# Optimization experiments

Hardware: AMD Instinct MI355X
Metric: run time of the kernel (lower is better)

The kernel has to match this reference:

```python
import jax, jax.numpy as jnp
import numpy as np

N = 100000   # nodes
E = 640000   # edges
F = 128      # num_features
D = 128      # dim
G = 128      # graphs in batch
BN_EPS = 1e-5


def setup_inputs() -> dict:
    key = jax.random.key(0)
    ks = jax.random.split(key, 16)
    lin = lambda k, i, o: (jax.random.normal(k, (i, o), jnp.float32) / np.sqrt(i)).astype(jnp.float32)
    inp = {
        "x": jax.random.normal(ks[0], (N, F), jnp.float32),
        "edge_index": jax.random.randint(ks[1], (2, E), 0, N),
        "batch": jnp.sort(jax.random.randint(ks[2], (N,), 0, G)),
        # layer 0: Linear(F,D)-ReLU-Linear(D,D), BN(D)
        "W0a": lin(ks[3], F, D), "b0a": jnp.zeros((D,), jnp.float32),
        "W0b": lin(ks[4], D, D), "b0b": jnp.zeros((D,), jnp.float32),
        "g0": jnp.ones((D,), jnp.float32), "be0": jnp.zeros((D,), jnp.float32),
        # layer 1: Linear(D,D)-ReLU-Linear(D,D), BN(D)
        "W1a": lin(ks[5], D, D), "b1a": jnp.zeros((D,), jnp.float32),
        "W1b": lin(ks[6], D, D), "b1b": jnp.zeros((D,), jnp.float32),
        "g1": jnp.ones((D,), jnp.float32), "be1": jnp.zeros((D,), jnp.float32),
        # layer 2: Linear(D,D)-ReLU-Linear(D,1), BN(1)
        "W2a": lin(ks[7], D, D), "b2a": jnp.zeros((D,), jnp.float32),
        "W2b": lin(ks[8], D, 1), "b2b": jnp.zeros((1,), jnp.float32),
        "g2": jnp.ones((1,), jnp.float32), "be2": jnp.zeros((1,), jnp.float32),
    }
    return inp


def _gin_layer(x, src, dst, Wa, ba, Wb, bb, g, be, relu_out):
    # GINConv (eps=0): h = x + sum_{j in N(i)} x_j, then MLP, then BN (train-mode stats)
    agg = jax.ops.segment_sum(x[src], dst, num_segments=N)
    h = x + agg
    h = jax.nn.relu(h @ Wa + ba) @ Wb + bb
    mu = jnp.mean(h, axis=0)
    var = jnp.mean((h - mu) ** 2, axis=0)  # biased var (torch BN normalization)
    h = (h - mu) * jax.lax.rsqrt(var + BN_EPS) * g + be
    return jax.nn.relu(h) if relu_out else h


def reference(x, edge_index, batch,
              W0a, b0a, W0b, b0b, g0, be0,
              W1a, b1a, W1b, b1b, g1, be1,
              W2a, b2a, W2b, b2b, g2, be2):
    src, dst = edge_index[0], edge_index[1]
    h = _gin_layer(x, src, dst, W0a, b0a, W0b, b0b, g0, be0, True)
    h = _gin_layer(h, src, dst, W1a, b1a, W1b, b1b, g1, be1, True)
    h = _gin_layer(h, src, dst, W2a, b2a, W2b, b2b, g2, be2, False)  # [N,1], no final ReLU
    # segment softmax over graphs, temperature 5.0 (PyG softmax semantics)
    z = h / 5.0
    m = jax.ops.segment_max(z, batch, num_segments=G)
    ez = jnp.exp(z - m[batch])
    s = jax.ops.segment_sum(ez, batch, num_segments=G)
    return ez / (s[batch] + 1e-16)
```

## Files before the change

kernel.cpp:

```cpp
#include <hip/hip_runtime.h>
#include <math.h>

#define NN 100000
#define EE 640000
#define GG 128
#define BN_EPS 1e-5f
#define NBLK 98

typedef __attribute__((ext_vector_type(8))) short short8;
typedef __attribute__((ext_vector_type(4))) float f32x4;


__device__ __forceinline__ short f2bf(float f) {
    unsigned u = __float_as_uint(f);
    u += 0x7fffu + ((u >> 16) & 1);
    return (short)(u >> 16);
}
__device__ __forceinline__ float bf2f(short s) {
    return __uint_as_float(((unsigned)(unsigned short)s) << 16);
}
__device__ __forceinline__ int swz(int row, int chunk) {
    return row * 128 + ((chunk ^ (row & 15)) << 3);
}
__device__ __forceinline__ int swze(int row, int col) {
    return row * 128 + (((col >> 3) ^ (row & 15)) << 3) + (col & 7);
}

__global__ void k_setup(const float* __restrict__ x,
                        const float* __restrict__ W0a, const float* __restrict__ W0b,
                        const float* __restrict__ W1a, const float* __restrict__ W1b,
                        const float* __restrict__ W2a, short* __restrict__ Wt,
                        short* __restrict__ Xbf, int* __restrict__ deg,
                        float* __restrict__ smf) {
    int idx = blockIdx.x * 256 + threadIdx.x;
    if (idx < 81920) {
        int wi = idx >> 14, r = idx & 16383;
        const float* W = (wi == 0) ? W0a : (wi == 1) ? W0b : (wi == 2) ? W1a
                        : (wi == 3) ? W1b : W2a;
        int k = r >> 7, n = r & 127;
        int ch = n >> 6, ct = (n >> 4) & 3, r16 = n & 15;
        int kc = k >> 3, kk = kc >> 2, q = kc & 3, e = k & 7;
        int lane = r16 + (q << 4);
        Wt[wi * 16384 + ((((ch * 4 + ct) * 4 + kk) * 64 + lane) << 3) + e] =
            f2bf(W[k * 128 + n]);
    }
    if (idx < NN) deg[idx] = 0;
    if (idx < 4112) smf[idx] = 0.0f;
    if (idx < 1600000) {
        const float4* xr = (const float4*)x + (size_t)idx * 2;
        float4 v0 = xr[0], v1 = xr[1];
        short8 o;
        o[0] = f2bf(v0.x); o[1] = f2bf(v0.y); o[2] = f2bf(v0.z); o[3] = f2bf(v0.w);
        o[4] = f2bf(v1.x); o[5] = f2bf(v1.y); o[6] = f2bf(v1.z); o[7] = f2bf(v1.w);
        *(short8*)(Xbf + (size_t)idx * 8) = o;
    }
}

__global__ void k_hist(const int* __restrict__ ei, int* __restrict__ deg) {
    int e = blockIdx.x * 256 + threadIdx.x;
    if (e < EE) atomicAdd(&deg[ei[EE + e]], 1);
}

__global__ __launch_bounds__(1024) void k_scan1(const int* __restrict__ deg,
                                                int* __restrict__ offs,
                                                int* __restrict__ bsums) {
    __shared__ int sm[1024];
    int t = threadIdx.x;
    int i = blockIdx.x * 1024 + t;
    int v = (i < NN) ? deg[i] : 0;
    sm[t] = v;
    __syncthreads();
    for (int off = 1; off < 1024; off <<= 1) {
        int add = (t >= off) ? sm[t - off] : 0;
        __syncthreads();
        sm[t] += add;
        __syncthreads();
    }
    if (i < NN) offs[i] = sm[t] - v;
    if (t == 1023) bsums[blockIdx.x] = sm[1023];
}

__global__ __launch_bounds__(1024) void k_scan3(int* __restrict__ offs,
                                                const int* __restrict__ bsums,
                                                int* __restrict__ pos) {
    __shared__ int smb[128];
    __shared__ int baseS;
    int t = threadIdx.x;
    if (t < 128) smb[t] = (t < NBLK) ? bsums[t] : 0;
    __syncthreads();
    if (t == 0) {
        int b = 0;
        for (int i = 0; i < (int)blockIdx.x; ++i) b += smb[i];
        baseS = b;
    }
    __syncthreads();
    int i = blockIdx.x * 1024 + t;
    if (i < NN) {
        int o = offs[i] + baseS;
        offs[i] = o;
        pos[i] = o;
    }
    if (i == 0) offs[NN] = EE;
}

__global__ void k_fill(const int* __restrict__ ei, int* __restrict__ pos,
                       int* __restrict__ csr) {
    int e = blockIdx.x * 256 + threadIdx.x;
    if (e < EE) {
        int d = ei[EE + e];
        int p = atomicAdd(&pos[d], 1);
        csr[p] = ei[e];
    }
}

template <int MODE>
__global__ __launch_bounds__(512, 4) void k_gmlp(const short* __restrict__ hin,
                                                 const int* __restrict__ offs,
                                                 const int* __restrict__ csr,
                                                 const float* __restrict__ rep,
                                                 const float* __restrict__ g,
                                                 const float* __restrict__ be,
                                                 const short* __restrict__ Wta,
                                                 const float* __restrict__ ba,
                                                 const short* __restrict__ Wtb,
                                                 const float* __restrict__ bb,
                                                 short* __restrict__ hout,
                                                 float* __restrict__ statsRep,
                                                 const float* __restrict__ w2,
                                                 const float* __restrict__ b2,
                                                 float* __restrict__ z,
                                                 float* __restrict__ s2rep) {
    __shared__ short Asb[16384];
    __shared__ float parS[128], parH[128];
    __shared__ float redS[1024];
    const int t = threadIdx.x;
    const int row0 = blockIdx.x * 128;
    const int lane = t & 63, wave = t >> 6;
    const int r16 = lane & 15, q = lane >> 4;
    const int rh = wave & 3, ch = wave >> 2;
    const int RA = rh * 32, CB = ch * 64;
    const int l = t & 15;

    if constexpr (MODE != 0) {
        if (t < 128) {
            float s = 0.f, ss = 0.f;
#pragma unroll
            for (int r = 0; r < 8; ++r) {
                s += rep[r * 256 + t];
                ss += rep[r * 256 + 128 + t];
            }
            const float inv = 1.0f / (float)NN;
            float mu = s * inv;
            float var = ss * inv - mu * mu;
            float sc = g[t] / sqrtf(var + BN_EPS);
            parS[t] = sc;
            parH[t] = be[t] - mu * sc;
        }
        __syncthreads();
    }

    const short* wA = Wta + (size_t)((ch * 1024 + lane) << 3);
    const short* wB = (MODE != 2) ? (Wtb + (size_t)((ch * 1024 + lane) << 3)) : nullptr;

    float sc8[8], sh8[8];
    if constexpr (MODE != 0) {
#pragma unroll
        for (int j = 0; j < 8; ++j) { sc8[j] = parS[l * 8 + j]; sh8[j] = parH[l * 8 + j]; }
    }
#pragma unroll
    for (int p = 0; p < 4; ++p) {
        int r = p * 32 + (t >> 4);
        int gr = row0 + r;
        float f8[8] = {0.f, 0.f, 0.f, 0.f, 0.f, 0.f, 0.f, 0.f};
        if (gr < NN) {
            int j0 = offs[gr], j1 = offs[gr + 1];
            short8 v = *(const short8*)(hin + (size_t)gr * 128 + l * 8);
#pragma unroll
            for (int k = 0; k < 8; ++k)
                f8[k] = (MODE != 0) ? fmaxf(fmaf(bf2f(v[k]), sc8[k], sh8[k]), 0.f) : bf2f(v[k]);
            int jlast = j1 - 1;
            for (int j = j0; j < j1; j += 4) {
                float m1 = (j + 1 <= jlast) ? 1.f : 0.f;
                float m2 = (j + 2 <= jlast) ? 1.f : 0.f;
                float m3 = (j + 3 <= jlast) ? 1.f : 0.f;
                int i1 = min(j + 1, jlast), i2 = min(j + 2, jlast), i3 = min(j + 3, jlast);
                int s0 = csr[j], s1 = csr[i1], s2 = csr[i2], s3 = csr[i3];
                short8 w0 = *(const short8*)(hin + (size_t)s0 * 128 + l * 8);
                short8 w1 = *(const short8*)(hin + (size_t)s1 * 128 + l * 8);
                short8 w2v = *(const short8*)(hin + (size_t)s2 * 128 + l * 8);
                short8 w3 = *(const short8*)(hin + (size_t)s3 * 128 + l * 8);
#pragma unroll
                for (int k = 0; k < 8; ++k) {
                    if constexpr (MODE != 0) {
                        f8[k] += fmaxf(fmaf(bf2f(w0[k]), sc8[k], sh8[k]), 0.f);
                        f8[k] = fmaf(m1, fmaxf(fmaf(bf2f(w1[k]), sc8[k], sh8[k]), 0.f), f8[k]);
                        f8[k] = fmaf(m2, fmaxf(fmaf(bf2f(w2v[k]), sc8[k], sh8[k]), 0.f), f8[k]);
                        f8[k] = fmaf(m3, fmaxf(fmaf(bf2f(w3[k]), sc8[k], sh8[k]), 0.f), f8[k]);
                    } else {
                        f8[k] += bf2f(w0[k]);
                        f8[k] = fmaf(m1, bf2f(w1[k]), f8[k]);
                        f8[k] = fmaf(m2, bf2f(w2v[k]), f8[k]);
                        f8[k] = fmaf(m3, bf2f(w3[k]), f8[k]);
                    }
                }
            }
        }
        short8 o;
#pragma unroll
        for (int k = 0; k < 8; ++k) o[k] = f2bf(f8[k]);
        *(short8*)&Asb[swz(r, l)] = o;
    }
    __syncthreads();

    f32x4 acc[2][4];
#pragma unroll
    for (int rt = 0; rt < 2; ++rt)
#pragma unroll
        for (int ct = 0; ct < 4; ++ct) acc[rt][ct] = (f32x4)0.f;
#pragma unroll
    for (int kk = 0; kk < 4; ++kk) {
        short8 b[4], a[2];
#pragma unroll
        for (int ct = 0; ct < 4; ++ct)
            b[ct] = *(const short8*)(wA + ((ct * 4 + kk) << 9));
#pragma unroll
        for (int rt = 0; rt < 2; ++rt)
            a[rt] = *(const short8*)&Asb[swz(RA + rt * 16 + r16, kk * 4 + q)];
#pragma unroll
        for (int rt = 0; rt < 2; ++rt)
#pragma unroll
            for (int ct = 0; ct < 4; ++ct)
                acc[rt][ct] = __builtin_amdgcn_mfma_f32_16x16x32_bf16(a[rt], b[ct], acc[rt][ct], 0, 0, 0);
    }
    __syncthreads();

    float bav[4];
#pragma unroll
    for (int ct = 0; ct < 4; ++ct) bav[ct] = ba[CB + ct * 16 + r16];
#pragma unroll
    for (int rt = 0; rt < 2; ++rt)
#pragma unroll
        for (int ct = 0; ct < 4; ++ct)
#pragma unroll
            for (int rg = 0; rg < 4; ++rg) {
                float m = fmaxf(acc[rt][ct][rg] + bav[ct], 0.f);
                Asb[swze(RA + rt * 16 + q * 4 + rg, CB + ct * 16 + r16)] = f2bf(m);
            }
    __syncthreads();

    if constexpr (MODE == 2) {
        const int rr = t >> 4;
        float4 w0 = ((const float4*)w2)[l * 2];
        float4 w1 = ((const float4*)w2)[l * 2 + 1];
        float b2v = b2[0];
        float s = 0.f, ss = 0.f;
#pragma unroll
        for (int p = 0; p < 4; ++p) {
            int r = p * 32 + rr;
            int gr = row0 + r;
            short8 v = *(const short8*)&Asb[swz(r, l)];
            float pp = bf2f(v[0]) * w0.x + bf2f(v[1]) * w0.y + bf2f(v[2]) * w0.z +
                       bf2f(v[3]) * w0.w + bf2f(v[4]) * w1.x + bf2f(v[5]) * w1.y +
                       bf2f(v[6]) * w1.z + bf2f(v[7]) * w1.w;
#pragma unroll
            for (int off = 1; off < 16; off <<= 1) pp += __shfl_xor(pp, off, 16);
            if (l == 0 && gr < NN) {
                float h2 = pp + b2v;
                z[gr] = h2;
                s += h2;
                ss += h2 * h2;
            }
        }
        s += __shfl_xor(s, 16); s += __shfl_xor(s, 32);
        ss += __shfl_xor(ss, 16); ss += __shfl_xor(ss, 32);
        if ((t & 63) == 0) { redS[wave * 2] = s; redS[wave * 2 + 1] = ss; }
        __syncthreads();
        if (t == 0) {
            float S = 0.f, SS = 0.f;
#pragma unroll
            for (int w = 0; w < 8; ++w) { S += redS[w * 2]; SS += redS[w * 2 + 1]; }
            int rp = (blockIdx.x & 7) * 2;
            unsafeAtomicAdd(&s2rep[rp], S);
            unsafeAtomicAdd(&s2rep[rp + 1], SS);
        }
        return;
    } else {
#pragma unroll
        for (int rt = 0; rt < 2; ++rt)
#pragma unroll
            for (int ct = 0; ct < 4; ++ct) acc[rt][ct] = (f32x4)0.f;
#pragma unroll
        for (int kk = 0; kk < 4; ++kk) {
            short8 b[4], a[2];
#pragma unroll
            for (int ct = 0; ct < 4; ++ct)
                b[ct] = *(const short8*)(wB + ((ct * 4 + kk) << 9));
#pragma unroll
            for (int rt = 0; rt < 2; ++rt)
                a[rt] = *(const short8*)&Asb[swz(RA + rt * 16 + r16, kk * 4 + q)];
#pragma unroll
            for (int rt = 0; rt < 2; ++rt)
#pragma unroll
                for (int ct = 0; ct < 4; ++ct)
                    acc[rt][ct] = __builtin_amdgcn_mfma_f32_16x16x32_bf16(a[rt], b[ct], acc[rt][ct], 0, 0, 0);
        }
        __syncthreads();

        float bbv[4];
#pragma unroll
        for (int ct = 0; ct < 4; ++ct) bbv[ct] = bb[CB + ct * 16 + r16];
        float s[4] = {0.f, 0.f, 0.f, 0.f}, ss[4] = {0.f, 0.f, 0.f, 0.f};
#pragma unroll
        for (int rt = 0; rt < 2; ++rt)
#pragma unroll
            for (int ct = 0; ct < 4; ++ct)
#pragma unroll
                for (int rg = 0; rg < 4; ++rg) {
                    int lr = RA + rt * 16 + q * 4 + rg;
                    int gr = row0 + lr;
                    float hv = acc[rt][ct][rg] + bbv[ct];
                    if (gr < NN) { s[ct] += hv; ss[ct] += hv * hv; }
                    Asb[swze(lr, CB + ct * 16 + r16)] = f2bf(hv);
                }
#pragma unroll
        for (int ct = 0; ct < 4; ++ct) {
            s[ct] += __shfl_xor(s[ct], 16);
            s[ct] += __shfl_xor(s[ct], 32);
            ss[ct] += __shfl_xor(ss[ct], 16);
            ss[ct] += __shfl_xor(ss[ct], 32);
        }
        if (lane < 16) {
#pragma unroll
            for (int ct = 0; ct < 4; ++ct) {
                int col = CB + ct * 16 + r16;
                redS[rh * 256 + col] = s[ct];
                redS[rh * 256 + 128 + col] = ss[ct];
            }
        }
        __syncthreads();
        if (t < 256) {
            float v = redS[t] + redS[256 + t] + redS[512 + t] + redS[768 + t];
            unsafeAtomicAdd(&statsRep[(blockIdx.x & 7) * 256 + t], v);
        }
#pragma unroll
        for (int i = 0; i < 4; ++i) {
            int f = i * 512 + t;
            int r = f >> 4, c8 = f & 15;
            int gr = row0 + r;
            if (gr < NN)
                *(short8*)(hout + (size_t)gr * 128 + c8 * 8) = *(const short8*)&Asb[swz(r, c8)];
        }
    }
}

__device__ __forceinline__ int lbound(const int* __restrict__ b, int val) {
    int lo = 0, hi = NN;
    while (lo < hi) {
        int m = (lo + hi) >> 1;
        if (b[m] < val) lo = m + 1; else hi = m;
    }
    return lo;
}

__global__ void k_softmax(const float* __restrict__ zr, const float* __restrict__ s2rep,
                          const float* __restrict__ g2, const float* __restrict__ be2,
                          const int* __restrict__ batch, float* __restrict__ out) {
    __shared__ float rb[4];
    const int g = blockIdx.x, t = threadIdx.x;
    const int lo = lbound(batch, g), hi = lbound(batch, g + 1);
    float s = 0.f, ssq = 0.f;
#pragma unroll
    for (int i = 0; i < 8; ++i) { s += s2rep[i * 2]; ssq += s2rep[i * 2 + 1]; }
    const float mu = s / (float)NN;
    const float var = ssq / (float)NN - mu * mu;
    const float sc = g2[0] / sqrtf(var + BN_EPS) * 0.2f;
    const float sh = (be2[0] - mu * g2[0] / sqrtf(var + BN_EPS)) * 0.2f;

    float m = -INFINITY;
    for (int i = lo + t; i < hi; i += 256) m = fmaxf(m, fmaf(zr[i], sc, sh));
#pragma unroll
    for (int off = 1; off < 64; off <<= 1) m = fmaxf(m, __shfl_xor(m, off, 64));
    if ((t & 63) == 0) rb[t >> 6] = m;
    __syncthreads();
    float gmax = fmaxf(fmaxf(rb[0], rb[1]), fmaxf(rb[2], rb[3]));
    __syncthreads();

    float sum = 0.f;
    for (int i = lo + t; i < hi; i += 256) {
        float e = expf(fmaf(zr[i], sc, sh) - gmax);
        out[i] = e;
        sum += e;
    }
#pragma unroll
    for (int off = 1; off < 64; off <<= 1) sum += __shfl_xor(sum, off, 64);
    if ((t & 63) == 0) rb[t >> 6] = sum;
    __syncthreads();
    float S = rb[0] + rb[1] + rb[2] + rb[3];
    float inv = 1.0f / (S + 1e-16f);
    for (int i = lo + t; i < hi; i += 256) out[i] *= inv;
}

extern "C" void kernel_launch(void* const* d_in, const int* in_sizes, int n_in,
                              void* d_out, int out_size, void* d_ws, size_t ws_size,
                              hipStream_t stream) {
    const float* x   = (const float*)d_in[0];
    const int* ei    = (const int*)d_in[1];
    const int* batch = (const int*)d_in[2];
    const float *W0a = (const float*)d_in[3],  *b0a = (const float*)d_in[4];
    const float *W0b = (const float*)d_in[5],  *b0b = (const float*)d_in[6];
    const float *g0  = (const float*)d_in[7],  *be0 = (const float*)d_in[8];
    const float *W1a = (const float*)d_in[9],  *b1a = (const float*)d_in[10];
    const float *W1b = (const float*)d_in[11], *b1b = (const float*)d_in[12];
    const float *g1  = (const float*)d_in[13], *be1 = (const float*)d_in[14];
    const float *W2a = (const float*)d_in[15], *b2a = (const float*)d_in[16];
    const float *W2b = (const float*)d_in[17], *b2b = (const float*)d_in[18];
    const float *g2  = (const float*)d_in[19], *be2 = (const float*)d_in[20];
    float* out = (float*)d_out;

    char* wsb = (char*)d_ws;
    short* Abf = (short*)wsb;
    short* Bbf = (short*)(wsb + 25600000);
    float* Zb  = (float*)(wsb + 51200000);
    float* SMf = (float*)(wsb + 51600000);
    float* S0r = SMf;
    float* S1r = SMf + 2048;
    float* S2r = SMf + 4096;
    int* offs  = (int*)(wsb + 51620000);
    int* bsums = (int*)(wsb + 52020004);
    int* csr   = (int*)(wsb + 52020516);
    short* Wt  = (short*)(wsb + 54580544);
    short* Xbf = (short*)(wsb + 54744384);
    int* deg = (int*)wsb;
    int* pos = (int*)(wsb + 400000);

    const int gE    = (EE + 255) / 256;
    const int gGmlp = (NN + 127) / 128;

    k_setup<<<6250, 256, 0, stream>>>(x, W0a, W0b, W1a, W1b, W2a, Wt, Xbf, deg, SMf);

    k_hist<<<gE, 256, 0, stream>>>(ei, deg);
    k_scan1<<<NBLK, 1024, 0, stream>>>(deg, offs, bsums);
    k_scan3<<<NBLK, 1024, 0, stream>>>(offs, bsums, pos);
    k_fill<<<gE, 256, 0, stream>>>(ei, pos, csr);

    k_gmlp<0><<<gGmlp, 512, 0, stream>>>(Xbf, offs, csr, nullptr, nullptr, nullptr,
                                         Wt, b0a, Wt + 16384, b0b, Abf, S0r,
                                         nullptr, nullptr, nullptr, nullptr);
    k_gmlp<1><<<gGmlp, 512, 0, stream>>>(Abf, offs, csr, S0r, g0, be0,
                                         Wt + 2 * 16384, b1a, Wt + 3 * 16384, b1b, Bbf, S1r,
                                         nullptr, nullptr, nullptr, nullptr);
    k_gmlp<2><<<gGmlp, 512, 0, stream>>>(Bbf, offs, csr, S1r, g1, be1,
                                         Wt + 4 * 16384, b2a, nullptr, nullptr,
                                         nullptr, nullptr, W2b, b2b, Zb, S2r);

    k_softmax<<<GG, 256, 0, stream>>>(Zb, S2r, g2, be2, batch, out);
}
```

Baseline: 361.1 us.

## Fuse CSR preprocessing into one cooperative kernel and widen gather unroll

Replaces five preprocessing launches (setup, histogram, two scan passes, fill) with a single cooperative kernel of 256x1024 threads that uses grid-wide syncs between phases. This cuts launch overhead and inter-kernel gaps. Separately, the neighbor-gather loop in the GIN MLP kernel is unrolled from 4 to 8 edges per iteration to put more loads in flight. The costs are grid.sync barriers, lower parallelism in the grid-stride phases, and more register pressure under launch_bounds(512,4).

```diff
diff --git a/kernel.cpp b/kernel.cpp
--- a/kernel.cpp
+++ b/kernel.cpp
@@ -1,5 +1,8 @@
 #include <hip/hip_runtime.h>
+#include <hip/hip_cooperative_groups.h>
 #include <math.h>
+
+namespace cg = cooperative_groups;
 
 #define NN 100000
 #define EE 640000
@@ -26,15 +29,32 @@
     return row * 128 + (((col >> 3) ^ (row & 15)) << 3) + (col & 7);
 }
 
-__global__ void k_setup(const float* __restrict__ x,
-                        const float* __restrict__ W0a, const float* __restrict__ W0b,
-                        const float* __restrict__ W1a, const float* __restrict__ W1b,
-                        const float* __restrict__ W2a, short* __restrict__ Wt,
-                        short* __restrict__ Xbf, int* __restrict__ deg,
-                        float* __restrict__ smf) {
-    int idx = blockIdx.x * 256 + threadIdx.x;
-    if (idx < 81920) {
-        int wi = idx >> 14, r = idx & 16383;
+__global__ __launch_bounds__(1024) void k_pre(
+        const float* __restrict__ x,
+        const float* __restrict__ W0a, const float* __restrict__ W0b,
+        const float* __restrict__ W1a, const float* __restrict__ W1b,
+        const float* __restrict__ W2a,
+        short* __restrict__ Wt, short* __restrict__ Xbf,
+        int* __restrict__ deg, float* __restrict__ smf,
+        const int* __restrict__ ei,
+        int* __restrict__ offs, int* __restrict__ bsums,
+        int* __restrict__ pos, int* __restrict__ csr) {
+    cg::grid_group grid = cg::this_grid();
+    __shared__ int sm[1024];
+    const int T = gridDim.x * blockDim.x;
+    const int tid = blockIdx.x * blockDim.x + threadIdx.x;
+    const int t = threadIdx.x;
+
+    for (int idx = tid; idx < 1600000; idx += T) {
+        const float4* xr = (const float4*)x + (size_t)idx * 2;
+        float4 v0 = xr[0], v1 = xr[1];
+        short8 o;
+        o[0] = f2bf(v0.x); o[1] = f2bf(v0.y); o[2] = f2bf(v0.z); o[3] = f2bf(v0.w);
+        o[4] = f2bf(v1.x); o[5] = f2bf(v1.y); o[6] = f2bf(v1.z); o[7] = f2bf(v1.w);
+        *(short8*)(Xbf + (size_t)idx * 8) = o;
+    }
+    if (tid < 81920) {
+        int wi = tid >> 14, r = tid & 16383;
         const float* W = (wi == 0) ? W0a : (wi == 1) ? W0b : (wi == 2) ? W1a
                         : (wi == 3) ? W1b : W2a;
         int k = r >> 7, n = r & 127;
@@ -44,69 +64,50 @@
         Wt[wi * 16384 + ((((ch * 4 + ct) * 4 + kk) * 64 + lane) << 3) + e] =
             f2bf(W[k * 128 + n]);
     }
-    if (idx < NN) deg[idx] = 0;
-    if (idx < 4112) smf[idx] = 0.0f;
-    if (idx < 1600000) {
-        const float4* xr = (const float4*)x + (size_t)idx * 2;
-        float4 v0 = xr[0], v1 = xr[1];
-        short8 o;
-        o[0] = f2bf(v0.x); o[1] = f2bf(v0.y); o[2] = f2bf(v0.z); o[3] = f2bf(v0.w);
-        o[4] = f2bf(v1.x); o[5] = f2bf(v1.y); o[6] = f2bf(v1.z); o[7] = f2bf(v1.w);
-        *(short8*)(Xbf + (size_t)idx * 8) = o;
-    }
-}
-
-__global__ void k_hist(const int* __restrict__ ei, int* __restrict__ deg) {
-    int e = blockIdx.x * 256 + threadIdx.x;
-    if (e < EE) atomicAdd(&deg[ei[EE + e]], 1);
-}
-
-__global__ __launch_bounds__(1024) void k_scan1(const int* __restrict__ deg,
-                                                int* __restrict__ offs,
-                                                int* __restrict__ bsums) {
-    __shared__ int sm[1024];
-    int t = threadIdx.x;
-    int i = blockIdx.x * 1024 + t;
-    int v = (i < NN) ? deg[i] : 0;
-    sm[t] = v;
-    __syncthreads();
-    for (int off = 1; off < 1024; off <<= 1) {
-        int add = (t >= off) ? sm[t - off] : 0;
-        __syncthreads();
-        sm[t] += add;
-        __syncthreads();
-    }
-    if (i < NN) offs[i] = sm[t] - v;
-    if (t == 1023) bsums[blockIdx.x] = sm[1023];
-}
-
-__global__ __launch_bounds__(1024) void k_scan3(int* __restrict__ offs,
-                                                const int* __restrict__ bsums,
-                                                int* __restrict__ pos) {
-    __shared__ int smb[128];
-    __shared__ int baseS;
-    int t = threadIdx.x;
-    if (t < 128) smb[t] = (t < NBLK) ? bsums[t] : 0;
-    __syncthreads();
-    if (t == 0) {
-        int b = 0;
-        for (int i = 0; i < (int)blockIdx.x; ++i) b += smb[i];
-        baseS = b;
-    }
-    __syncthreads();
-    int i = blockIdx.x * 1024 + t;
-    if (i < NN) {
-        int o = offs[i] + baseS;
-        offs[i] = o;
-        pos[i] = o;
-    }
-    if (i == 0) offs[NN] = EE;
-}
-
-__global__ void k_fill(const int* __restrict__ ei, int* __restrict__ pos,
-                       int* __restrict__ csr) {
-    int e = blockIdx.x * 256 + threadIdx.x;
-    if (e < EE) {
+    if (tid < NN) deg[tid] = 0;
+    if (tid < 4112) smf[tid] = 0.0f;
+    grid.sync();
+
+    for (int e = tid; e < EE; e += T) atomicAdd(&deg[ei[EE + e]], 1);
+    grid.sync();
+
+    if (blockIdx.x < NBLK) {
+        int i = blockIdx.x * 1024 + t;
+        int v = (i < NN) ? deg[i] : 0;
+        sm[t] = v;
+        __syncthreads();
+        for (int off = 1; off < 1024; off <<= 1) {
+            int add = (t >= off) ? sm[t - off] : 0;
+            __syncthreads();
+            sm[t] += add;
+            __syncthreads();
+        }
+        if (i < NN) offs[i] = sm[t] - v;
+        if (t == 1023) bsums[blockIdx.x] = sm[1023];
+    }
+    grid.sync();
+
+    if (blockIdx.x < NBLK) {
+        if (t < 128) sm[t] = (t < NBLK) ? bsums[t] : 0;
+        __syncthreads();
+        if (t == 0) {
+            int b = 0;
+            for (int i = 0; i < (int)blockIdx.x; ++i) b += sm[i];
+            sm[512] = b;
+        }
+        __syncthreads();
+        int base = sm[512];
+        int i = blockIdx.x * 1024 + t;
+        if (i < NN) {
+            int o = offs[i] + base;
+            offs[i] = o;
+            pos[i] = o;
+        }
+    }
+    if (tid == 0) offs[NN] = EE;
+    grid.sync();
+
+    for (int e = tid; e < EE; e += T) {
         int d = ei[EE + e];
         int p = atomicAdd(&pos[d], 1);
         csr[p] = ei[e];
@@ -179,28 +180,35 @@
             for (int k = 0; k < 8; ++k)
                 f8[k] = (MODE != 0) ? fmaxf(fmaf(bf2f(v[k]), sc8[k], sh8[k]), 0.f) : bf2f(v[k]);
             int jlast = j1 - 1;
-            for (int j = j0; j < j1; j += 4) {
-                float m1 = (j + 1 <= jlast) ? 1.f : 0.f;
-                float m2 = (j + 2 <= jlast) ? 1.f : 0.f;
-                float m3 = (j + 3 <= jlast) ? 1.f : 0.f;
-                int i1 = min(j + 1, jlast), i2 = min(j + 2, jlast), i3 = min(j + 3, jlast);
-                int s0 = csr[j], s1 = csr[i1], s2 = csr[i2], s3 = csr[i3];
-                short8 w0 = *(const short8*)(hin + (size_t)s0 * 128 + l * 8);
-                short8 w1 = *(const short8*)(hin + (size_t)s1 * 128 + l * 8);
-                short8 w2v = *(const short8*)(hin + (size_t)s2 * 128 + l * 8);
-                short8 w3 = *(const short8*)(hin + (size_t)s3 * 128 + l * 8);
+            for (int j = j0; j < j1; j += 8) {
+                int ii[8];
+                float mk[8];
+                ii[0] = j;
+                mk[0] = 1.f;
+#pragma unroll
+                for (int u = 1; u < 8; ++u) {
+                    ii[u] = min(j + u, jlast);
+                    mk[u] = (j + u <= jlast) ? 1.f : 0.f;
+                }
+                int sidx[8];
+#pragma unroll
+                for (int u = 0; u < 8; ++u) sidx[u] = csr[ii[u]];
+                short8 w[8];
+#pragma unroll
+                for (int u = 0; u < 8; ++u)
+                    w[u] = *(const short8*)(hin + (size_t)sidx[u] * 128 + l * 8);
 #pragma unroll
                 for (int k = 0; k < 8; ++k) {
                     if constexpr (MODE != 0) {
-                        f8[k] += fmaxf(fmaf(bf2f(w0[k]), sc8[k], sh8[k]), 0.f);
-                        f8[k] = fmaf(m1, fmaxf(fmaf(bf2f(w1[k]), sc8[k], sh8[k]), 0.f), f8[k]);
-                        f8[k] = fmaf(m2, fmaxf(fmaf(bf2f(w2v[k]), sc8[k], sh8[k]), 0.f), f8[k]);
-                        f8[k] = fmaf(m3, fmaxf(fmaf(bf2f(w3[k]), sc8[k], sh8[k]), 0.f), f8[k]);
+                        f8[k] += fmaxf(fmaf(bf2f(w[0][k]), sc8[k], sh8[k]), 0.f);
+#pragma unroll
+                        for (int u = 1; u < 8; ++u)
+                            f8[k] = fmaf(mk[u], fmaxf(fmaf(bf2f(w[u][k]), sc8[k], sh8[k]), 0.f), f8[k]);
                     } else {
-                        f8[k] += bf2f(w0[k]);
-                        f8[k] = fmaf(m1, bf2f(w1[k]), f8[k]);
-                        f8[k] = fmaf(m2, bf2f(w2v[k]), f8[k]);
-                        f8[k] = fmaf(m3, bf2f(w3[k]), f8[k]);
+                        f8[k] += bf2f(w[0][k]);
+#pragma unroll
+                        for (int u = 1; u < 8; ++u)
+                            f8[k] = fmaf(mk[u], bf2f(w[u][k]), f8[k]);
                     }
                 }
             }
@@ -433,15 +441,15 @@
     int* deg = (int*)wsb;
     int* pos = (int*)(wsb + 400000);
 
-    const int gE    = (EE + 255) / 256;
     const int gGmlp = (NN + 127) / 128;
 
-    k_setup<<<6250, 256, 0, stream>>>(x, W0a, W0b, W1a, W1b, W2a, Wt, Xbf, deg, SMf);
-
-    k_hist<<<gE, 256, 0, stream>>>(ei, deg);
-    k_scan1<<<NBLK, 1024, 0, stream>>>(deg, offs, bsums);
-    k_scan3<<<NBLK, 1024, 0, stream>>>(offs, bsums, pos);
-    k_fill<<<gE, 256, 0, stream>>>(ei, pos, csr);
+    void* preArgs[] = {
+        (void*)&x, (void*)&W0a, (void*)&W0b, (void*)&W1a, (void*)&W1b, (void*)&W2a,
+        (void*)&Wt, (void*)&Xbf, (void*)&deg, (void*)&SMf,
+        (void*)&ei, (void*)&offs, (void*)&bsums, (void*)&pos, (void*)&csr
+    };
+    hipLaunchCooperativeKernel((const void*)k_pre, dim3(256), dim3(1024),
+                               preArgs, 0, stream);
 
     k_gmlp<0><<<gGmlp, 512, 0, stream>>>(Xbf, offs, csr, nullptr, nullptr, nullptr,
                                          Wt, b0a, Wt + 16384, b0b, Abf, S0r,
```

New measurement: 551.7 us. 1.53x slower.

## Halve GIN block tile to 64 rows and widen neighbor gather unroll to 8

Applied to the files above, without the earlier changes.

The fused gather+MLP kernel now processes 64 rows per 256-thread block instead of 128 rows per 512-thread block, doubling grid size and halving LDS per block. This aims at better load balance and occupancy across CUs. The neighbor aggregation loop is also unrolled from 4 to 8 edges per iteration, so more independent gather loads are in flight. The cost is higher register pressure, extra masked work on low-degree nodes, and more per-block weight reloads and stats atomics.

```diff
diff --git a/kernel.cpp b/kernel.cpp
--- a/kernel.cpp
+++ b/kernel.cpp
@@ -114,7 +114,7 @@
 }
 
 template <int MODE>
-__global__ __launch_bounds__(512, 4) void k_gmlp(const short* __restrict__ hin,
+__global__ __launch_bounds__(256, 4) void k_gmlp(const short* __restrict__ hin,
                                                  const int* __restrict__ offs,
                                                  const int* __restrict__ csr,
                                                  const float* __restrict__ rep,
@@ -130,14 +130,14 @@
                                                  const float* __restrict__ b2,
                                                  float* __restrict__ z,
                                                  float* __restrict__ s2rep) {
-    __shared__ short Asb[16384];
+    __shared__ short Asb[8192];
     __shared__ float parS[128], parH[128];
     __shared__ float redS[1024];
     const int t = threadIdx.x;
-    const int row0 = blockIdx.x * 128;
+    const int row0 = blockIdx.x * 64;
     const int lane = t & 63, wave = t >> 6;
     const int r16 = lane & 15, q = lane >> 4;
-    const int rh = wave & 3, ch = wave >> 2;
+    const int rh = wave & 1, ch = wave >> 1;
     const int RA = rh * 32, CB = ch * 64;
     const int l = t & 15;
 
@@ -169,7 +169,7 @@
     }
 #pragma unroll
     for (int p = 0; p < 4; ++p) {
-        int r = p * 32 + (t >> 4);
+        int r = p * 16 + (t >> 4);
         int gr = row0 + r;
         float f8[8] = {0.f, 0.f, 0.f, 0.f, 0.f, 0.f, 0.f, 0.f};
         if (gr < NN) {
@@ -179,28 +179,35 @@
             for (int k = 0; k < 8; ++k)
                 f8[k] = (MODE != 0) ? fmaxf(fmaf(bf2f(v[k]), sc8[k], sh8[k]), 0.f) : bf2f(v[k]);
             int jlast = j1 - 1;
-            for (int j = j0; j < j1; j += 4) {
-                float m1 = (j + 1 <= jlast) ? 1.f : 0.f;
-                float m2 = (j + 2 <= jlast) ? 1.f : 0.f;
-                float m3 = (j + 3 <= jlast) ? 1.f : 0.f;
-                int i1 = min(j + 1, jlast), i2 = min(j + 2, jlast), i3 = min(j + 3, jlast);
-                int s0 = csr[j], s1 = csr[i1], s2 = csr[i2], s3 = csr[i3];
-                short8 w0 = *(const short8*)(hin + (size_t)s0 * 128 + l * 8);
-                short8 w1 = *(const short8*)(hin + (size_t)s1 * 128 + l * 8);
-                short8 w2v = *(const short8*)(hin + (size_t)s2 * 128 + l * 8);
-                short8 w3 = *(const short8*)(hin + (size_t)s3 * 128 + l * 8);
+            for (int j = j0; j < j1; j += 8) {
+                int ii[8];
+                float mk[8];
+                ii[0] = j;
+                mk[0] = 1.f;
+#pragma unroll
+                for (int u = 1; u < 8; ++u) {
+                    ii[u] = min(j + u, jlast);
+                    mk[u] = (j + u <= jlast) ? 1.f : 0.f;
+                }
+                int sidx[8];
+#pragma unroll
+                for (int u = 0; u < 8; ++u) sidx[u] = csr[ii[u]];
+                short8 w[8];
+#pragma unroll
+                for (int u = 0; u < 8; ++u)
+                    w[u] = *(const short8*)(hin + (size_t)sidx[u] * 128 + l * 8);
 #pragma unroll
                 for (int k = 0; k < 8; ++k) {
                     if constexpr (MODE != 0) {
-                        f8[k] += fmaxf(fmaf(bf2f(w0[k]), sc8[k], sh8[k]), 0.f);
-                        f8[k] = fmaf(m1, fmaxf(fmaf(bf2f(w1[k]), sc8[k], sh8[k]), 0.f), f8[k]);
-                        f8[k] = fmaf(m2, fmaxf(fmaf(bf2f(w2v[k]), sc8[k], sh8[k]), 0.f), f8[k]);
-                        f8[k] = fmaf(m3, fmaxf(fmaf(bf2f(w3[k]), sc8[k], sh8[k]), 0.f), f8[k]);
+                        f8[k] += fmaxf(fmaf(bf2f(w[0][k]), sc8[k], sh8[k]), 0.f);
+#pragma unroll
+                        for (int u = 1; u < 8; ++u)
+                            f8[k] = fmaf(mk[u], fmaxf(fmaf(bf2f(w[u][k]), sc8[k], sh8[k]), 0.f), f8[k]);
                     } else {
-                        f8[k] += bf2f(w0[k]);
-                        f8[k] = fmaf(m1, bf2f(w1[k]), f8[k]);
-                        f8[k] = fmaf(m2, bf2f(w2v[k]), f8[k]);
-                        f8[k] = fmaf(m3, bf2f(w3[k]), f8[k]);
+                        f8[k] += bf2f(w[0][k]);
+#pragma unroll
+                        for (int u = 1; u < 8; ++u)
+                            f8[k] = fmaf(mk[u], bf2f(w[u][k]), f8[k]);
                     }
                 }
             }
@@ -256,7 +263,7 @@
         float s = 0.f, ss = 0.f;
 #pragma unroll
         for (int p = 0; p < 4; ++p) {
-            int r = p * 32 + rr;
+            int r = p * 16 + rr;
             int gr = row0 + r;
             short8 v = *(const short8*)&Asb[swz(r, l)];
             float pp = bf2f(v[0]) * w0.x + bf2f(v[1]) * w0.y + bf2f(v[2]) * w0.z +
@@ -278,7 +285,7 @@
         if (t == 0) {
             float S = 0.f, SS = 0.f;
 #pragma unroll
-            for (int w = 0; w < 8; ++w) { S += redS[w * 2]; SS += redS[w * 2 + 1]; }
+            for (int w = 0; w < 4; ++w) { S += redS[w * 2]; SS += redS[w * 2 + 1]; }
             int rp = (blockIdx.x & 7) * 2;
             unsafeAtomicAdd(&s2rep[rp], S);
             unsafeAtomicAdd(&s2rep[rp + 1], SS);
@@ -333,18 +340,18 @@
 #pragma unroll
             for (int ct = 0; ct < 4; ++ct) {
                 int col = CB + ct * 16 + r16;
-                redS[rh * 256 + col] = s[ct];
-                redS[rh * 256 + 128 + col] = ss[ct];
+                redS[rh * 512 + col] = s[ct];
+                redS[rh * 512 + 128 + col] = ss[ct];
             }
         }
         __syncthreads();
         if (t < 256) {
-            float v = redS[t] + redS[256 + t] + redS[512 + t] + redS[768 + t];
+            float v = redS[t] + redS[512 + t];
             unsafeAtomicAdd(&statsRep[(blockIdx.x & 7) * 256 + t], v);
         }
 #pragma unroll
         for (int i = 0; i < 4; ++i) {
-            int f = i * 512 + t;
+            int f = i * 256 + t;
             int r = f >> 4, c8 = f & 15;
             int gr = row0 + r;
             if (gr < NN)
@@ -434,7 +441,7 @@
     int* pos = (int*)(wsb + 400000);
 
     const int gE    = (EE + 255) / 256;
-    const int gGmlp = (NN + 127) / 128;
+    const int gGmlp = (NN + 63) / 64;
 
     k_setup<<<6250, 256, 0, stream>>>(x, W0a, W0b, W1a, W1b, W2a, Wt, Xbf, deg, SMf);
 
@@ -443,13 +450,13 @@
     k_scan3<<<NBLK, 1024, 0, stream>>>(offs, bsums, pos);
     k_fill<<<gE, 256, 0, stream>>>(ei, pos, csr);
 
-    k_gmlp<0><<<gGmlp, 512, 0, stream>>>(Xbf, offs, csr, nullptr, nullptr, nullptr,
+    k_gmlp<0><<<gGmlp, 256, 0, stream>>>(Xbf, offs, csr, nullptr, nullptr, nullptr,
                                          Wt, b0a, Wt + 16384, b0b, Abf, S0r,
                                          nullptr, nullptr, nullptr, nullptr);
-    k_gmlp<1><<<gGmlp, 512, 0, stream>>>(Abf, offs, csr, S0r, g0, be0,
+    k_gmlp<1><<<gGmlp, 256, 0, stream>>>(Abf, offs, csr, S0r, g0, be0,
                                          Wt + 2 * 16384, b1a, Wt + 3 * 16384, b1b, Bbf, S1r,
                                          nullptr, nullptr, nullptr, nullptr);
-    k_gmlp<2><<<gGmlp, 512, 0, stream>>>(Bbf, offs, csr, S1r, g1, be1,
+    k_gmlp<2><<<gGmlp, 256, 0, stream>>>(Bbf, offs, csr, S1r, g1, be1,
                                          Wt + 4 * 16384, b2a, nullptr, nullptr,
                                          nullptr, nullptr, W2b, b2b, Zb, S2r);
 
```

After: 385.6 us. 6.8% more time.

## Fuse histogram into prep kernel, narrow gather lanes, raise gmlp occupancy

Applied to the files above, without the earlier changes.

Merges the degree histogram into the x-to-bf16 conversion kernel and replaces the in-kernel zeroing of deg and stats with memset calls. In the GIN layer kernels, the neighbor gather now uses 32 lanes per row with 4 bf16 values each (8-byte loads) and 16 rows per pass, instead of 16 lanes with 8 values each. The launch-bounds minimum-blocks hint is raised from 4 to 6 to allow more resident blocks. The narrower loads give more rows in flight per wave and more memory-level parallelism for the gather, at the cost of smaller transactions and possible register pressure or spills under the tighter bound.

```diff
diff --git a/kernel.cpp b/kernel.cpp
--- a/kernel.cpp
+++ b/kernel.cpp
@@ -8,6 +8,7 @@
 #define NBLK 98
 
 typedef __attribute__((ext_vector_type(8))) short short8;
+typedef __attribute__((ext_vector_type(4))) short bhalf4;
 typedef __attribute__((ext_vector_type(4))) float f32x4;
 
 
@@ -26,13 +27,22 @@
     return row * 128 + (((col >> 3) ^ (row & 15)) << 3) + (col & 7);
 }
 
-__global__ void k_setup(const float* __restrict__ x,
-                        const float* __restrict__ W0a, const float* __restrict__ W0b,
-                        const float* __restrict__ W1a, const float* __restrict__ W1b,
-                        const float* __restrict__ W2a, short* __restrict__ Wt,
-                        short* __restrict__ Xbf, int* __restrict__ deg,
-                        float* __restrict__ smf) {
+__global__ void k_prep(const float* __restrict__ x,
+                       const float* __restrict__ W0a, const float* __restrict__ W0b,
+                       const float* __restrict__ W1a, const float* __restrict__ W1b,
+                       const float* __restrict__ W2a, short* __restrict__ Wt,
+                       short* __restrict__ Xbf, const int* __restrict__ ei,
+                       int* __restrict__ deg) {
     int idx = blockIdx.x * 256 + threadIdx.x;
+    if (idx < 1600000) {
+        const float4* xr = (const float4*)x + (size_t)idx * 2;
+        float4 v0 = xr[0], v1 = xr[1];
+        short8 o;
+        o[0] = f2bf(v0.x); o[1] = f2bf(v0.y); o[2] = f2bf(v0.z); o[3] = f2bf(v0.w);
+        o[4] = f2bf(v1.x); o[5] = f2bf(v1.y); o[6] = f2bf(v1.z); o[7] = f2bf(v1.w);
+        *(short8*)(Xbf + (size_t)idx * 8) = o;
+    }
+    if (idx < EE) atomicAdd(&deg[ei[EE + idx]], 1);
     if (idx < 81920) {
         int wi = idx >> 14, r = idx & 16383;
         const float* W = (wi == 0) ? W0a : (wi == 1) ? W0b : (wi == 2) ? W1a
@@ -44,21 +54,6 @@
         Wt[wi * 16384 + ((((ch * 4 + ct) * 4 + kk) * 64 + lane) << 3) + e] =
             f2bf(W[k * 128 + n]);
     }
-    if (idx < NN) deg[idx] = 0;
-    if (idx < 4112) smf[idx] = 0.0f;
-    if (idx < 1600000) {
-        const float4* xr = (const float4*)x + (size_t)idx * 2;
-        float4 v0 = xr[0], v1 = xr[1];
-        short8 o;
-        o[0] = f2bf(v0.x); o[1] = f2bf(v0.y); o[2] = f2bf(v0.z); o[3] = f2bf(v0.w);
-        o[4] = f2bf(v1.x); o[5] = f2bf(v1.y); o[6] = f2bf(v1.z); o[7] = f2bf(v1.w);
-        *(short8*)(Xbf + (size_t)idx * 8) = o;
-    }
-}
-
-__global__ void k_hist(const int* __restrict__ ei, int* __restrict__ deg) {
-    int e = blockIdx.x * 256 + threadIdx.x;
-    if (e < EE) atomicAdd(&deg[ei[EE + e]], 1);
 }
 
 __global__ __launch_bounds__(1024) void k_scan1(const int* __restrict__ deg,
@@ -114,7 +109,7 @@
 }
 
 template <int MODE>
-__global__ __launch_bounds__(512, 4) void k_gmlp(const short* __restrict__ hin,
+__global__ __launch_bounds__(512, 6) void k_gmlp(const short* __restrict__ hin,
                                                  const int* __restrict__ offs,
                                                  const int* __restrict__ csr,
                                                  const float* __restrict__ rep,
@@ -139,7 +134,9 @@
     const int r16 = lane & 15, q = lane >> 4;
     const int rh = wave & 3, ch = wave >> 2;
     const int RA = rh * 32, CB = ch * 64;
-    const int l = t & 15;
+    const int l16 = t & 15;
+    const int gl = t & 31;
+    const int nrow = t >> 5;
 
     if constexpr (MODE != 0) {
         if (t < 128) {
@@ -162,53 +159,55 @@
     const short* wA = Wta + (size_t)((ch * 1024 + lane) << 3);
     const short* wB = (MODE != 2) ? (Wtb + (size_t)((ch * 1024 + lane) << 3)) : nullptr;
 
-    float sc8[8], sh8[8];
+    float sc4[4], sh4[4];
     if constexpr (MODE != 0) {
 #pragma unroll
-        for (int j = 0; j < 8; ++j) { sc8[j] = parS[l * 8 + j]; sh8[j] = parH[l * 8 + j]; }
-    }
-#pragma unroll
-    for (int p = 0; p < 4; ++p) {
-        int r = p * 32 + (t >> 4);
+        for (int j = 0; j < 4; ++j) { sc4[j] = parS[gl * 4 + j]; sh4[j] = parH[gl * 4 + j]; }
+    }
+#pragma unroll
+    for (int p = 0; p < 8; ++p) {
+        int r = p * 16 + nrow;
         int gr = row0 + r;
-        float f8[8] = {0.f, 0.f, 0.f, 0.f, 0.f, 0.f, 0.f, 0.f};
+        float f4[4] = {0.f, 0.f, 0.f, 0.f};
         if (gr < NN) {
             int j0 = offs[gr], j1 = offs[gr + 1];
-            short8 v = *(const short8*)(hin + (size_t)gr * 128 + l * 8);
-#pragma unroll
-            for (int k = 0; k < 8; ++k)
-                f8[k] = (MODE != 0) ? fmaxf(fmaf(bf2f(v[k]), sc8[k], sh8[k]), 0.f) : bf2f(v[k]);
+            bhalf4 v = *(const bhalf4*)(hin + (size_t)gr * 128 + gl * 4);
+#pragma unroll
+            for (int k = 0; k < 4; ++k)
+                f4[k] = (MODE != 0) ? fmaxf(fmaf(bf2f(v[k]), sc4[k], sh4[k]), 0.f) : bf2f(v[k]);
             int jlast = j1 - 1;
             for (int j = j0; j < j1; j += 4) {
                 float m1 = (j + 1 <= jlast) ? 1.f : 0.f;
                 float m2 = (j + 2 <= jlast) ? 1.f : 0.f;
                 float m3 = (j + 3 <= jlast) ? 1.f : 0.f;
-                int i1 = min(j + 1, jlast), i2 = min(j + 2, jlast), i3 = min(j + 3, jlast);
-                int s0 = csr[j], s1 = csr[i1], s2 = csr[i2], s3 = csr[i3];
-                short8 w0 = *(const short8*)(hin + (size_t)s0 * 128 + l * 8);
-                short8 w1 = *(const short8*)(hin + (size_t)s1 * 128 + l * 8);
-                short8 w2v = *(const short8*)(hin + (size_t)s2 * 128 + l * 8);
-                short8 w3 = *(const short8*)(hin + (size_t)s3 * 128 + l * 8);
-#pragma unroll
-                for (int k = 0; k < 8; ++k) {
+                int s0 = csr[j];
+                int s1 = csr[min(j + 1, jlast)];
+                int s2 = csr[min(j + 2, jlast)];
+                int s3 = csr[min(j + 3, jlast)];
+                bhalf4 w0 = *(const bhalf4*)(hin + (size_t)s0 * 128 + gl * 4);
+                bhalf4 w1 = *(const bhalf4*)(hin + (size_t)s1 * 128 + gl * 4);
+                bhalf4 w2v = *(const bhalf4*)(hin + (size_t)s2 * 128 + gl * 4);
+                bhalf4 w3 = *(const bhalf4*)(hin + (size_t)s3 * 128 + gl * 4);
+#pragma unroll
+                for (int k = 0; k < 4; ++k) {
                     if constexpr (MODE != 0) {
-                        f8[k] += fmaxf(fmaf(bf2f(w0[k]), sc8[k], sh8[k]), 0.f);
-                        f8[k] = fmaf(m1, fmaxf(fmaf(bf2f(w1[k]), sc8[k], sh8[k]), 0.f), f8[k]);
-                        f8[k] = fmaf(m2, fmaxf(fmaf(bf2f(w2v[k]), sc8[k], sh8[k]), 0.f), f8[k]);
-                        f8[k] = fmaf(m3, fmaxf(fmaf(bf2f(w3[k]), sc8[k], sh8[k]), 0.f), f8[k]);
+                        f4[k] += fmaxf(fmaf(bf2f(w0[k]), sc4[k], sh4[k]), 0.f);
+                        f4[k] = fmaf(m1, fmaxf(fmaf(bf2f(w1[k]), sc4[k], sh4[k]), 0.f), f4[k]);
+                        f4[k] = fmaf(m2, fmaxf(fmaf(bf2f(w2v[k]), sc4[k], sh4[k]), 0.f), f4[k]);
+                        f4[k] = fmaf(m3, fmaxf(fmaf(bf2f(w3[k]), sc4[k], sh4[k]), 0.f), f4[k]);
                     } else {
-                        f8[k] += bf2f(w0[k]);
-                        f8[k] = fmaf(m1, bf2f(w1[k]), f8[k]);
-                        f8[k] = fmaf(m2, bf2f(w2v[k]), f8[k]);
-                        f8[k] = fmaf(m3, bf2f(w3[k]), f8[k]);
+                        f4[k] += bf2f(w0[k]);
+                        f4[k] = fmaf(m1, bf2f(w1[k]), f4[k]);
+                        f4[k] = fmaf(m2, bf2f(w2v[k]), f4[k]);
+                        f4[k] = fmaf(m3, bf2f(w3[k]), f4[k]);
                     }
                 }
             }
         }
-        short8 o;
-#pragma unroll
-        for (int k = 0; k < 8; ++k) o[k] = f2bf(f8[k]);
-        *(short8*)&Asb[swz(r, l)] = o;
+        bhalf4 o;
+#pragma unroll
+        for (int k = 0; k < 4; ++k) o[k] = f2bf(f4[k]);
+        *(bhalf4*)&Asb[swze(r, gl * 4)] = o;
     }
     __syncthreads();
 
@@ -250,21 +249,21 @@
 
     if constexpr (MODE == 2) {
         const int rr = t >> 4;
-        float4 w0 = ((const float4*)w2)[l * 2];
-        float4 w1 = ((const float4*)w2)[l * 2 + 1];
+        float4 w0 = ((const float4*)w2)[l16 * 2];
+        float4 w1 = ((const float4*)w2)[l16 * 2 + 1];
         float b2v = b2[0];
         float s = 0.f, ss = 0.f;
 #pragma unroll
         for (int p = 0; p < 4; ++p) {
             int r = p * 32 + rr;
             int gr = row0 + r;
-            short8 v = *(const short8*)&Asb[swz(r, l)];
+            short8 v = *(const short8*)&Asb[swz(r, l16)];
             float pp = bf2f(v[0]) * w0.x + bf2f(v[1]) * w0.y + bf2f(v[2]) * w0.z +
                        bf2f(v[3]) * w0.w + bf2f(v[4]) * w1.x + bf2f(v[5]) * w1.y +
                        bf2f(v[6]) * w1.z + bf2f(v[7]) * w1.w;
 #pragma unroll
             for (int off = 1; off < 16; off <<= 1) pp += __shfl_xor(pp, off, 16);
-            if (l == 0 && gr < NN) {
+            if (l16 == 0 && gr < NN) {
                 float h2 = pp + b2v;
                 z[gr] = h2;
                 s += h2;
@@ -436,9 +435,11 @@
     const int gE    = (EE + 255) / 256;
     const int gGmlp = (NN + 127) / 128;
 
-    k_setup<<<6250, 256, 0, stream>>>(x, W0a, W0b, W1a, W1b, W2a, Wt, Xbf, deg, SMf);
-
-    k_hist<<<gE, 256, 0, stream>>>(ei, deg);
+    (void)hipMemsetAsync(deg, 0, NN * sizeof(int), stream);
+    (void)hipMemsetAsync(SMf, 0, 4112 * sizeof(float), stream);
+
+    k_prep<<<6400, 256, 0, stream>>>(x, W0a, W0b, W1a, W1b, W2a, Wt, Xbf, ei, deg);
+
     k_scan1<<<NBLK, 1024, 0, stream>>>(deg, offs, bsums);
     k_scan3<<<NBLK, 1024, 0, stream>>>(offs, bsums, pos);
     k_fill<<<gE, 256, 0, stream>>>(ei, pos, csr);
```

After: 431.9 us. +19.6%, slower.
